# Kernel tuning notes

Hardware: AMD Instinct MI355X
Metric: run time of the kernel (lower is better)

## Reference

```python
import jax, jax.numpy as jnp
import numpy as np

D, T1, T2, T3 = 1024, 256, 128, 64
IV2, IV3, BUF = 16, 128, 32
B, T = 16, 1024

_PARAM_SHAPES = {
    "w_t1g": (D + T1, T1), "b_t1g": (T1,),
    "w_t1c": (D + T1, T1), "b_t1c": (T1,),
    "w_t1r": (T1, D), "b_t1r": (D,),
    "w_t2v": (D, T2), "b_t2v": (T2,),
    "w_t2b": (D, 1), "b_t2b": (1,),
    "w_t2r": (T2, D), "b_t2r": (D,),
    "w_t3o": (D, T3), "b_t3o": (T3,),
    "w_t3n": (D, T3), "b_t3n": (T3,),
    "w_t3r": (2 * T3, D), "b_t3r": (D,),
    "w_b32": (T3, T2), "b_b32": (T2,),
    "w_b21": (T2, T1), "b_b21": (T1,),
    "w_fuse": (3 * D, D), "b_fuse": (D,),
}

def setup_inputs() -> dict:
    key = jax.random.key(0)
    inp = {"x": jax.random.normal(jax.random.fold_in(key, 0), (B, T, D), jnp.float32)}
    for i, (name, shape) in enumerate(_PARAM_SHAPES.items()):
        inp[name] = 0.02 * jax.random.normal(jax.random.fold_in(key, i + 1), shape, jnp.float32)
    inp["ln_g"] = jnp.ones((D,), jnp.float32)
    inp["ln_b"] = jnp.zeros((D,), jnp.float32)
    return inp

def reference(x, w_t1g, b_t1g, w_t1c, b_t1c, w_t1r, b_t1r, w_t2v, b_t2v, w_t2b, b_t2b, w_t2r, b_t2r, w_t3o, b_t3o, w_t3n, b_t3n, w_t3r, b_t3r, w_b32, b_b32, w_b21, b_b21, w_fuse, b_fuse, ln_g, ln_b):
    Bsz, Tlen, _ = x.shape
    tier1 = jnp.zeros((Bsz, T1), x.dtype)
    tier2 = jnp.zeros((Bsz, T2), x.dtype)
    tier3 = jnp.zeros((Bsz, T3), x.dtype)
    var3 = jnp.ones((Bsz, T3), x.dtype)
    buf = jnp.zeros((Bsz, BUF, D), x.dtype)  # consolidation buffer

    def step(carry, inp_t):
        tier1, tier2, tier3, var3, buf = carry
        x_t, tc = inp_t  # tc = token_count (1-indexed)
        # cross-tier broadcasts
        bias21 = jnp.tanh(tier2 @ w_b21 + b_b21)
        bias32 = jnp.tanh(tier3 @ w_b32 + b_b32)
        # tier1: GRU-style gated update
        t1b = tier1 + bias21
        comb = jnp.concatenate([x_t, t1b], axis=-1)
        gate = jax.nn.sigmoid(comb @ w_t1g + b_t1g)
        cand = jnp.tanh(comb @ w_t1c + b_t1c)
        tier1 = gate * t1b + (1.0 - gate) * cand
        read1 = tier1 @ w_t1r + b_t1r
        # tier2: delta-rule overwrite every IV2 tokens (buffer mean BEFORE this token is written)
        do2 = (tc % IV2) == 0
        bm = buf.mean(axis=1)
        t2b = tier2 + bias32
        v = bm @ w_t2v + b_t2v
        beta = jax.nn.sigmoid(bm @ w_t2b + b_t2b)
        tier2 = jnp.where(do2, t2b + beta * (v - t2b), tier2)
        read2 = tier2 @ w_t2r + b_t2r
        # tier3: diagonal Kalman update every IV3 tokens, observation = tier2 readout
        do3 = (tc % IV3) == 0
        z = read2 @ w_t3o + b_t3o
        r = jax.nn.softplus(read2 @ w_t3n + b_t3n) + 0.01
        sp = 0.99 * var3 + 0.01
        K = sp / (sp + r + 1e-8)
        tier3 = jnp.where(do3, tier3 + K * (z - tier3), tier3)
        var3 = jnp.where(do3, (1.0 - K) * sp, var3)
        read3 = jnp.concatenate([tier3, var3], axis=-1) @ w_t3r + b_t3r
        fused = jnp.concatenate([read1, read2, read3], axis=-1) @ w_fuse + b_fuse
        # ring-buffer write (detached in torch -> stop_gradient)
        idx = (tc - 1) % BUF
        buf = jax.lax.dynamic_update_slice(buf, jax.lax.stop_gradient(x_t)[:, None, :], (0, idx, 0))
        return (tier1, tier2, tier3, var3, buf), fused

    tcs = jnp.arange(1, Tlen + 1, dtype=jnp.int32)
    _, ys = jax.lax.scan(step, (tier1, tier2, tier3, var3, buf), (jnp.swapaxes(x, 0, 1), tcs))
    out = jnp.swapaxes(ys, 0, 1)  # [B, T, D]
    mu = out.mean(-1, keepdims=True)
    xc = out - mu
    return xc * jax.lax.rsqrt(jnp.mean(xc * xc, -1, keepdims=True) + 1e-5) * ln_g + ln_b
```

## Files before the change

kernel.cpp:

```cpp
#include <hip/hip_runtime.h>

#define D_ 1024
#define T_ 1024
#define B_ 16

typedef short s16x8 __attribute__((ext_vector_type(8)));
typedef float f32x4 __attribute__((ext_vector_type(4)));

__device__ __forceinline__ unsigned short bf16_rne(float f){
  unsigned int u = __builtin_bit_cast(unsigned int, f);
  u += 0x7FFFu + ((u >> 16) & 1u);
  return (unsigned short)(u >> 16);
}
__device__ __forceinline__ float bf16_tof(unsigned short h){
  unsigned int u = ((unsigned int)h) << 16;
  return __builtin_bit_cast(float, u);
}
__device__ __forceinline__ float fsig(float x){ return 1.0f/(1.0f+__expf(-x)); }
__device__ __forceinline__ float ftanh(float x){ return 2.0f*fsig(2.0f*x)-1.0f; }

template <typename V>
__device__ __forceinline__ auto mfma_try(V a, V b, f32x4 c, int)
    -> decltype(__builtin_amdgcn_mfma_f32_16x16x32_bf16(a, b, c, 0, 0, 0)) {
  return __builtin_amdgcn_mfma_f32_16x16x32_bf16(a, b, c, 0, 0, 0);
}
template <typename V>
__device__ __forceinline__ f32x4 mfma_try(V a, V b, f32x4 c, long) {
  typedef __bf16 bf16x8 __attribute__((ext_vector_type(8)));
  return __builtin_amdgcn_mfma_f32_16x16x32_bf16(
      __builtin_bit_cast(bf16x8, a), __builtin_bit_cast(bf16x8, b), c, 0, 0, 0);
}
__device__ __forceinline__ f32x4 MFMA(s16x8 a, s16x8 b, f32x4 c){
  return mfma_try(a, b, c, 0);
}


__device__ __forceinline__ void dev_conv4(const float* __restrict__ s,
                                          unsigned short* __restrict__ d, int g){
  float4 v = *(const float4*)(s + (size_t)g*4);
  ushort4 o; o.x=bf16_rne(v.x); o.y=bf16_rne(v.y); o.z=bf16_rne(v.z); o.w=bf16_rne(v.w);
  *(ushort4*)(d + (size_t)g*4) = o;
}

__device__ __forceinline__ void dev_fragprep(const float* __restrict__ w, int rowOff,
                                             int KT, int Nsrc,
                                             unsigned short* __restrict__ dst, int slot){
  int lane = slot & 63; int tmp = slot >> 6; int kt = tmp % KT; int nt = tmp / KT;
  int kbase = kt*32 + (lane>>4)*8; int col = nt*16 + (lane&15);
  unsigned short* o = dst + (size_t)slot*8;
  #pragma unroll
  for (int j=0;j<8;j++) o[j] = bf16_rne(w[(size_t)(rowOff + kbase + j)*Nsrc + col]);
}

__device__ __forceinline__ void dev_bm(const float* __restrict__ x,
                                       unsigned short* __restrict__ bm, int blk, int tid){
  int e = blk >> 4; int b = blk & 15;
  int tc = 16*(e+1); int hi = tc-2; int lo = tc-33; if (lo < 0) lo = 0;
  const float* xb = x + (size_t)b*T_*D_;
  for (int d = tid; d < D_; d += 256){
    float s = 0.f;
    for (int ss = lo; ss <= hi; ++ss) s += xb[(size_t)ss*D_ + d];
    bm[((size_t)(e*16+b))*D_ + d] = bf16_rne(s * (1.0f/32.0f));
  }
}

__device__ __forceinline__ void dev_bconst(const float* __restrict__ wf, const float* __restrict__ bf,
                                           const float* __restrict__ b1, const float* __restrict__ b2,
                                           const float* __restrict__ b3, float* __restrict__ bc,
                                           int blk, int tid){
  __shared__ float part[4][64];
  int n = blk*64 + (tid&63);
  int sl = tid>>6;
  float s = 0.f;
  for (int k=sl*256; k<(sl+1)*256; ++k){
    s += b1[k]*wf[(size_t)k*1024+n] + b2[k]*wf[(size_t)(1024+k)*1024+n] + b3[k]*wf[(size_t)(2048+k)*1024+n];
  }
  part[sl][tid&63] = s; __syncthreads();
  if (sl==0) bc[n] = bf[n] + part[0][tid] + part[1][tid] + part[2][tid] + part[3][tid];
}

__device__ __forceinline__ void dev_b2(const float* __restrict__ b_t2r, const float* __restrict__ w3o,
                                       const float* __restrict__ b3o, const float* __restrict__ w3n,
                                       const float* __restrict__ b3n, float* __restrict__ b2o,
                                       float* __restrict__ b2n, int tid){
  __shared__ float part[2][128];
  int idx = tid & 127; int sl = tid >> 7;
  int mat = idx>>6, n = idx&63;
  const float* w = mat ? w3n : w3o;
  float s = 0.f;
  for (int k=sl*512; k<(sl+1)*512; ++k) s += b_t2r[k]*w[(size_t)k*64+n];
  part[sl][idx] = s; __syncthreads();
  if (sl==0){
    float r = part[0][idx] + part[1][idx] + (mat? b3n[n] : b3o[n]);
    if (mat) b2n[n] = r; else b2o[n] = r;
  }
}

__device__ __forceinline__ void dev_gemm(int M, int K,
    const unsigned short* __restrict__ A, int lda,
    const unsigned short* __restrict__ Bf,
    const float* __restrict__ bias, int act,
    float* __restrict__ C, int ldc, int cb, int rb, int tid){
  int KT = K >> 5;
  int w = tid >> 6, l = tid & 63;
  int rbase = rb*64 + w*16;
  int arow = rbase + (l & 15); if (arow >= M) arow = M-1;
  const unsigned short* Aptr = A + (size_t)arow*lda + ((l>>4)*8);
  const s16x8* B0 = (const s16x8*)Bf + ((size_t)(cb*4+0)*KT)*64 + l;
  const s16x8* B1 = (const s16x8*)Bf + ((size_t)(cb*4+1)*KT)*64 + l;
  const s16x8* B2 = (const s16x8*)Bf + ((size_t)(cb*4+2)*KT)*64 + l;
  const s16x8* B3 = (const s16x8*)Bf + ((size_t)(cb*4+3)*KT)*64 + l;
  f32x4 z = {0.f,0.f,0.f,0.f};
  f32x4 acc0=z, acc1=z, acc2=z, acc3=z;
  for (int kt=0; kt<KT; ++kt){
    s16x8 a = *(const s16x8*)(Aptr + (size_t)kt*32);
    acc0 = MFMA(a, B0[(size_t)kt*64], acc0);
    acc1 = MFMA(a, B1[(size_t)kt*64], acc1);
    acc2 = MFMA(a, B2[(size_t)kt*64], acc2);
    acc3 = MFMA(a, B3[(size_t)kt*64], acc3);
  }
  int r0 = (l>>4)*4;
  #pragma unroll
  for (int i=0;i<4;i++){
    f32x4 acc = i==0?acc0 : i==1?acc1 : i==2?acc2 : acc3;
    int col = (cb*4+i)*16 + (l&15);
    float bs = bias ? bias[col] : 0.0f;
    #pragma unroll
    for (int j=0;j<4;j++){
      int row = rbase + r0 + j;
      if (row < M){
        float vv = acc[j] + bs;
        if (act==1) vv = ftanh(vv);
        C[(size_t)row*ldc + col] = vv;
      }
    }
  }
}

__device__ void dev_traj(
    const float* __restrict__ v, const float* __restrict__ beta,
    const float* __restrict__ w_b32, const float* __restrict__ b_b32,
    const float* __restrict__ w2o, const float* __restrict__ b2o,
    const float* __restrict__ w2n, const float* __restrict__ b2n,
    unsigned short* __restrict__ t2traj, unsigned short* __restrict__ t3traj, int tid){
  __shared__ float t2[16*128];
  __shared__ float t3[16*64];
  __shared__ float var3[16*64];
  __shared__ float zb[16*64];
  __shared__ float rb[16*64];
  for (int i=tid;i<2048;i+=1024){ t2[i]=0.f; t2traj[i]=0; }
  for (int i=tid;i<1024;i+=1024){
    int b=i>>6, n=i&63;
    t3[i]=0.f; var3[i]=1.f;
    t3traj[(size_t)b*128 + n] = 0;
    t3traj[(size_t)b*128 + 64 + n] = bf16_rne(1.f);
  }
  __syncthreads();
  for (int k=1;k<=64;k++){
    for (int i=tid;i<2048;i+=1024){
      int b=i>>7, n=i&127;
      float s=b_b32[n];
      for (int j=0;j<64;j++) s += t3[b*64+j]*w_b32[j*128+n];
      float t2b = t2[i] + ftanh(s);
      float bt = beta[(k-1)*16+b];
      float nv = t2b + bt*(v[(size_t)((k-1)*16+b)*128+n] - t2b);
      t2[i]=nv;
      t2traj[((size_t)k*16+b)*128+n] = bf16_rne(nv);
    }
    if ((k&7)==0){
      __syncthreads();
      for (int i=tid;i<2048;i+=1024){
        int mat=i>>10, b=(i>>6)&15, n=i&63;
        const float* w = mat? w2n : w2o;
        float s = mat? b2n[n] : b2o[n];
        for (int j=0;j<128;j++) s += t2[b*128+j]*w[j*64+n];
        if (mat){ float r = (s>20.f)? s : log1pf(__expf(s)); rb[b*64+n]=r+0.01f; }
        else zb[b*64+n]=s;
      }
      __syncthreads();
      for (int i=tid;i<1024;i+=1024){
        int b=i>>6, n=i&63;
        float sp = 0.99f*var3[i]+0.01f;
        float Kk = sp/(sp+rb[i]+1e-8f);
        float t3n_ = t3[i] + Kk*(zb[i]-t3[i]);
        float v3n = (1.f-Kk)*sp;
        t3[i]=t3n_; var3[i]=v3n;
        int jj=k>>3;
        t3traj[((size_t)jj*16+b)*128+n]    = bf16_rne(t3n_);
        t3traj[((size_t)jj*16+b)*128+64+n] = bf16_rne(v3n);
      }
      __syncthreads();
    }
  }
}


__global__ __launch_bounds__(256) void k_f1(
    const float* __restrict__ x, unsigned short* __restrict__ xtb,
    const float* __restrict__ w_t1r, unsigned short* __restrict__ w_t1r_bf,
    const float* __restrict__ w_t2r, unsigned short* __restrict__ w_t2r_bf,
    const float* __restrict__ w_t3r, unsigned short* __restrict__ w_t3r_bf,
    const float* __restrict__ w_t1g, const float* __restrict__ w_t1c,
    unsigned short* __restrict__ wgc1f, unsigned short* __restrict__ wg2f,
    unsigned short* __restrict__ wc2f,
    const float* __restrict__ w_t2v, unsigned short* __restrict__ wtvf,
    const float* __restrict__ w_b21, unsigned short* __restrict__ wb21f,
    const float* __restrict__ w_fuse, unsigned short* __restrict__ wf1f,
    unsigned short* __restrict__ wf2f, unsigned short* __restrict__ wf3f,
    const float* __restrict__ w_t3o, unsigned short* __restrict__ w3of,
    const float* __restrict__ w_t3n, unsigned short* __restrict__ w3nf,
    unsigned short* __restrict__ bm,
    const float* __restrict__ b_fuse, const float* __restrict__ b_t1r,
    const float* __restrict__ b_t2r, const float* __restrict__ b_t3r,
    float* __restrict__ bconst,
    const float* __restrict__ b_t3o, const float* __restrict__ b_t3n,
    float* __restrict__ b2o, float* __restrict__ b2n,
    const float* __restrict__ b_t1g, const float* __restrict__ b_t1c,
    float* __restrict__ bgc){
  int blk = blockIdx.x, tid = threadIdx.x;
  if (blk < 1024){
    for (int i=0;i<16;i++){
      int r = blk*16 + i; int b = r & 15, t = r >> 4; int d = tid*4;
      float4 v = *(const float4*)(x + ((size_t)b*T_ + t)*D_ + d);
      ushort4 o; o.x=bf16_rne(v.x); o.y=bf16_rne(v.y); o.z=bf16_rne(v.z); o.w=bf16_rne(v.w);
      *(ushort4*)(xtb + (size_t)r*D_ + d) = o;
    }
  } else if (blk < 1280){ dev_conv4(w_t1r, w_t1r_bf, (blk-1024)*256 + tid); }
  else if (blk < 1408){ dev_conv4(w_t2r, w_t2r_bf, (blk-1280)*256 + tid); }
  else if (blk < 1536){ dev_conv4(w_t3r, w_t3r_bf, (blk-1408)*256 + tid); }
  else if (blk < 1664){ dev_fragprep(w_t1g, 0, 32, 256, wgc1f,          (blk-1536)*256 + tid); }
  else if (blk < 1792){ dev_fragprep(w_t1c, 0, 32, 256, wgc1f + 262144, (blk-1664)*256 + tid); }
  else if (blk < 1824){ dev_fragprep(w_t1g, 1024, 8, 256, wg2f, (blk-1792)*256 + tid); }
  else if (blk < 1856){ dev_fragprep(w_t1c, 1024, 8, 256, wc2f, (blk-1824)*256 + tid); }
  else if (blk < 1920){ dev_fragprep(w_t2v, 0, 32, 128, wtvf, (blk-1856)*256 + tid); }
  else if (blk < 1936){ dev_fragprep(w_b21, 0, 4, 256, wb21f, (blk-1920)*256 + tid); }
  else if (blk < 2448){ dev_fragprep(w_fuse, 0,    32, 1024, wf1f, (blk-1936)*256 + tid); }
  else if (blk < 2960){ dev_fragprep(w_fuse, 1024, 32, 1024, wf2f, (blk-2448)*256 + tid); }
  else if (blk < 3472){ dev_fragprep(w_fuse, 2048, 32, 1024, wf3f, (blk-2960)*256 + tid); }
  else if (blk < 3504){ dev_fragprep(w_t3o, 0, 32, 64, w3of, (blk-3472)*256 + tid); }
  else if (blk < 3536){ dev_fragprep(w_t3n, 0, 32, 64, w3nf, (blk-3504)*256 + tid); }
  else if (blk < 4560){ dev_bm(x, bm, blk-3536, tid); }
  else if (blk < 4576){ dev_bconst(w_fuse, b_fuse, b_t1r, b_t2r, b_t3r, bconst, blk-4560, tid); }
  else if (blk < 4577){ dev_b2(b_t2r, w_t3o, b_t3o, w_t3n, b_t3n, b2o, b2n, tid); }
  else { bgc[tid] = b_t1g[tid]; bgc[256+tid] = b_t1c[tid]; }
}

__global__ __launch_bounds__(256) void k_f2(
    const unsigned short* __restrict__ xtb, const unsigned short* __restrict__ wgc1f,
    const float* __restrict__ bgc, float* __restrict__ P,
    const unsigned short* __restrict__ bm, const unsigned short* __restrict__ wtvf,
    const float* __restrict__ b_t2v, float* __restrict__ v,
    const unsigned short* __restrict__ w_t1r_bf, const unsigned short* __restrict__ wf1f,
    float* __restrict__ wr1f,
    const unsigned short* __restrict__ w_t2r_bf, const unsigned short* __restrict__ wf2f,
    float* __restrict__ wr2f,
    const unsigned short* __restrict__ w_t3r_bf, const unsigned short* __restrict__ wf3f,
    float* __restrict__ wr3f,
    const unsigned short* __restrict__ w3of, float* __restrict__ w2o,
    const unsigned short* __restrict__ w3nf, float* __restrict__ w2n,
    const float* __restrict__ w_t2b, const float* __restrict__ b_t2b,
    float* __restrict__ beta){
  int blk = blockIdx.x, tid = threadIdx.x;
  if (blk < 2048){ int r = blk;        dev_gemm(16384, 1024, xtb, 1024, wgc1f, bgc, 0, P, 512, r&7, r>>3, tid); }
  else if (blk < 2080){ int r = blk-2048; dev_gemm(1024, 1024, bm, 1024, wtvf, b_t2v, 0, v, 128, r&1, r>>1, tid); }
  else if (blk < 2144){ int r = blk-2080; dev_gemm(256, 1024, w_t1r_bf, 1024, wf1f, nullptr, 0, wr1f, 1024, r&15, r>>4, tid); }
  else if (blk < 2176){ int r = blk-2144; dev_gemm(128, 1024, w_t2r_bf, 1024, wf2f, nullptr, 0, wr2f, 1024, r&15, r>>4, tid); }
  else if (blk < 2208){ int r = blk-2176; dev_gemm(128, 1024, w_t3r_bf, 1024, wf3f, nullptr, 0, wr3f, 1024, r&15, r>>4, tid); }
  else if (blk < 2210){ int r = blk-2208; dev_gemm(128, 1024, w_t2r_bf, 1024, w3of, nullptr, 0, w2o, 64, 0, r, tid); }
  else if (blk < 2212){ int r = blk-2210; dev_gemm(128, 1024, w_t2r_bf, 1024, w3nf, nullptr, 0, w2n, 64, 0, r, tid); }
  else {
    int rel = blk-2212;
    int r = rel*4 + (tid>>6), l = tid&63;
    float s = 0.f;
    for (int d=l; d<D_; d+=64) s += bf16_tof(bm[(size_t)r*D_+d]) * w_t2b[d];
    #pragma unroll
    for (int off=32; off; off>>=1) s += __shfl_down(s, off);
    if (l==0) beta[r] = fsig(s + b_t2b[0]);
  }
}

__global__ __launch_bounds__(1024) void k_f3(
    const float* __restrict__ wr1f, unsigned short* __restrict__ wr1ff,
    const float* __restrict__ wr2f, unsigned short* __restrict__ wr2ff,
    const float* __restrict__ wr3f, unsigned short* __restrict__ wr3ff,
    const float* __restrict__ v, const float* __restrict__ beta,
    const float* __restrict__ w_b32, const float* __restrict__ b_b32,
    const float* __restrict__ w2o, const float* __restrict__ b2o,
    const float* __restrict__ w2n, const float* __restrict__ b2n,
    unsigned short* __restrict__ t2traj, unsigned short* __restrict__ t3traj){
  int blk = blockIdx.x, tid = threadIdx.x;
  if (blk < 32){ dev_fragprep(wr1f, 0, 8, 1024, wr1ff, blk*1024 + tid); }
  else if (blk < 48){ dev_fragprep(wr2f, 0, 4, 1024, wr2ff, (blk-32)*1024 + tid); }
  else if (blk < 64){ dev_fragprep(wr3f, 0, 4, 1024, wr3ff, (blk-48)*1024 + tid); }
  else { dev_traj(v, beta, w_b32, b_b32, w2o, b2o, w2n, b2n, t2traj, t3traj, tid); }
}

__global__ __launch_bounds__(256) void k_f4(
    const unsigned short* __restrict__ t2traj, const unsigned short* __restrict__ wb21f,
    const float* __restrict__ b_b21, float* __restrict__ b21seg,
    const unsigned short* __restrict__ wr2ff, float* __restrict__ f2seg,
    const unsigned short* __restrict__ t3traj, const unsigned short* __restrict__ wr3ff,
    float* __restrict__ f3seg){
  int blk = blockIdx.x, tid = threadIdx.x;
  if (blk < 68){ int r = blk;      dev_gemm(1040, 128, t2traj, 128, wb21f, b_b21, 1, b21seg, 256, r&3, r>>2, tid); }
  else if (blk < 340){ int r = blk-68;  dev_gemm(1040, 128, t2traj, 128, wr2ff, nullptr, 0, f2seg, 1024, r&15, r>>4, tid); }
  else {               int r = blk-340; dev_gemm(144, 128, t3traj, 128, wr3ff, nullptr, 0, f3seg, 1024, r&15, r>>4, tid); }
}

__global__ __launch_bounds__(512) void k_recur(
    const float* __restrict__ P,
    const float* __restrict__ b21,
    const unsigned short* __restrict__ Wg2f, const unsigned short* __restrict__ Wc2f,
    unsigned short* __restrict__ traj){
  __shared__ unsigned short sbuf[2][256];
  int b = blockIdx.x;
  int tid = threadIdx.x, w = tid>>6, l = tid&63;
  int hi = l>>4, cl = l&15;
  const s16x8* Bg = (const s16x8*)Wg2f;
  const s16x8* Bc = (const s16x8*)Wc2f;
  s16x8 bg0[8], bg1[8], bc0[8], bc1[8];
  #pragma unroll
  for (int kt=0;kt<8;kt++){
    bg0[kt] = Bg[((size_t)(2*w)*8  +kt)*64 + l];
    bg1[kt] = Bg[((size_t)(2*w+1)*8+kt)*64 + l];
    bc0[kt] = Bc[((size_t)(2*w)*8  +kt)*64 + l];
    bc1[kt] = Bc[((size_t)(2*w+1)*8+kt)*64 + l];
  }
  bool owner = (hi < 2);
  int nt = 2*w + hi;
  int n  = nt*16 + cl;
  if (!owner) n = 2*w*16 + cl;
  float t1b = 0.f;
  float pgN=0.f, pcN=0.f, bbN=0.f;
  if (owner){
    bbN = b21[((size_t)b)*256 + n];
    t1b = bbN;
    pgN = P[((size_t)b)*512 + n];
    pcN = P[((size_t)b)*512 + 256 + n];
    sbuf[0][n] = bf16_rne(t1b);
  }
  asm volatile("s_waitcnt lgkmcnt(0)\ns_barrier" ::: "memory");
  for (int t=0;t<1024;t++){
    float pg = pgN, pc = pcN, bb = bbN;
    int tn = (t+1 < 1024) ? (t+1) : 1023;
    if (owner){
      pgN = P[((size_t)(tn*16+b))*512 + n];
      pcN = P[((size_t)(tn*16+b))*512 + 256 + n];
      bbN = b21[(((size_t)((t+2)>>4))*16 + b)*256 + n];
    }
    const unsigned short* sb = sbuf[t&1];
    f32x4 z = {0.f,0.f,0.f,0.f};
    f32x4 ag0=z, ag1=z, ac0=z, ac1=z;
    #pragma unroll
    for (int kt=0;kt<8;kt++){
      s16x8 a = *(const s16x8*)(sb + kt*32 + hi*8);
      ag0 = MFMA(a, bg0[kt], ag0);
      ag1 = MFMA(a, bg1[kt], ag1);
      ac0 = MFMA(a, bc0[kt], ac0);
      ac1 = MFMA(a, bc1[kt], ac1);
    }
    if (owner){
      float gacc = (hi==0)? ag0[0] : ag1[0];
      float cacc = (hi==0)? ac0[0] : ac1[0];
      float g = fsig(gacc + pg);
      float c = ftanh(cacc + pc);
      float t1n = g*t1b + (1.f-g)*c;
      traj[((size_t)(t*16+b))*256 + n] = bf16_rne(t1n);
      t1b = t1n + bb;
      sbuf[(t+1)&1][n] = bf16_rne(t1b);
    }
    asm volatile("s_waitcnt lgkmcnt(0)\ns_barrier" ::: "memory");
  }
}

__global__ __launch_bounds__(1024) void k_final(
    const unsigned short* __restrict__ traj, const unsigned short* __restrict__ Bf,
    const float* __restrict__ bconst, const float* __restrict__ f2seg, const float* __restrict__ f3seg,
    const float* __restrict__ ln_g, const float* __restrict__ ln_b, float* __restrict__ out){
  __shared__ float buf[16*1024];
  __shared__ float mu[16];
  __shared__ float rs[16];
  int t = blockIdx.x, tid = threadIdx.x, w = tid>>6, l = tid&63;
  const unsigned short* Ab = traj + ((size_t)t*16 + (l&15))*256 + (l>>4)*8;
  const s16x8* Bp = (const s16x8*)Bf;
  f32x4 z = {0.f,0.f,0.f,0.f};
  f32x4 ac[4]; ac[0]=z; ac[1]=z; ac[2]=z; ac[3]=z;
  #pragma unroll
  for (int kt=0;kt<8;kt++){
    s16x8 a = *(const s16x8*)(Ab + kt*32);
    #pragma unroll
    for (int i=0;i<4;i++){
      int nt = w*4+i;
      ac[i] = MFMA(a, Bp[((size_t)nt*8+kt)*64+l], ac[i]);
    }
  }
  int tc = t+1, s2 = tc>>4, s3 = tc>>7;
  int r0 = (l>>4)*4, cl = l&15;
  #pragma unroll
  for (int i=0;i<4;i++){
    int col = (w*4+i)*16+cl;
    #pragma unroll
    for (int j=0;j<4;j++){
      int b = r0+j;
      buf[b*1024+col] = ac[i][j] + bconst[col]
        + f2seg[((size_t)s2*16+b)*1024+col] + f3seg[((size_t)s3*16+b)*1024+col];
    }
  }
  __syncthreads();
  {
    float s=0.f, q=0.f;
    #pragma unroll
    for (int i=0;i<16;i++){ float xv = buf[w*1024 + l + 64*i]; s+=xv; q+=xv*xv; }
    #pragma unroll
    for (int off=32;off;off>>=1){ s += __shfl_down(s,off); q += __shfl_down(q,off); }
    if (l==0){ float m = s*(1.f/1024.f); float var = q*(1.f/1024.f) - m*m; mu[w]=m; rs[w]=rsqrtf(var+1e-5f); }
  }
  __syncthreads();
  {
    int b = tid>>6, d0 = tid&63;
    float m = mu[b], r = rs[b];
    size_t ob = ((size_t)b*1024 + t)*1024;
    #pragma unroll
    for (int i=0;i<16;i++){
      int d = d0 + 64*i;
      out[ob + d] = (buf[b*1024+d]-m)*r*ln_g[d] + ln_b[d];
    }
  }
}

extern "C" void kernel_launch(void* const* d_in, const int* in_sizes, int n_in,
                              void* d_out, int out_size, void* d_ws, size_t ws_size,
                              hipStream_t stream){
  const float* x     = (const float*)d_in[0];
  const float* w_t1g = (const float*)d_in[1];
  const float* b_t1g = (const float*)d_in[2];
  const float* w_t1c = (const float*)d_in[3];
  const float* b_t1c = (const float*)d_in[4];
  const float* w_t1r = (const float*)d_in[5];
  const float* b_t1r = (const float*)d_in[6];
  const float* w_t2v = (const float*)d_in[7];
  const float* b_t2v = (const float*)d_in[8];
  const float* w_t2b = (const float*)d_in[9];
  const float* b_t2b = (const float*)d_in[10];
  const float* w_t2r = (const float*)d_in[11];
  const float* b_t2r = (const float*)d_in[12];
  const float* w_t3o = (const float*)d_in[13];
  const float* b_t3o = (const float*)d_in[14];
  const float* w_t3n = (const float*)d_in[15];
  const float* b_t3n = (const float*)d_in[16];
  const float* w_t3r = (const float*)d_in[17];
  const float* b_t3r = (const float*)d_in[18];
  const float* w_b32 = (const float*)d_in[19];
  const float* b_b32 = (const float*)d_in[20];
  const float* w_b21 = (const float*)d_in[21];
  const float* b_b21 = (const float*)d_in[22];
  const float* w_fuse= (const float*)d_in[23];
  const float* b_fuse= (const float*)d_in[24];
  const float* ln_g  = (const float*)d_in[25];
  const float* ln_b  = (const float*)d_in[26];
  float* out = (float*)d_out;
  (void)in_sizes; (void)n_in; (void)out_size; (void)ws_size;

  char* base = (char*)d_ws;
  size_t off = 0;
  auto alloc = [&](size_t bytes) -> void* {
    void* p = base + off;
    off += (bytes + 255) & ~(size_t)255;
    return p;
  };
  unsigned short* xtb   = (unsigned short*)alloc((size_t)B_*T_*D_*2);
  float* P              = (float*)alloc((size_t)B_*T_*512*4);
  unsigned short* traj1 = (unsigned short*)alloc((size_t)B_*T_*256*2);
  unsigned short* bm    = (unsigned short*)alloc((size_t)1024*1024*2);
  float* v      = (float*)alloc((size_t)1024*128*4);
  float* beta   = (float*)alloc(1024*4);
  float* wr1f   = (float*)alloc((size_t)256*1024*4);
  float* wr2f   = (float*)alloc((size_t)128*1024*4);
  float* wr3f   = (float*)alloc((size_t)128*1024*4);
  float* w2o    = (float*)alloc(128*64*4);
  float* w2n    = (float*)alloc(128*64*4);
  float* b2o    = (float*)alloc(64*4);
  float* b2n    = (float*)alloc(64*4);
  float* bconst = (float*)alloc(1024*4);
  float* bgc    = (float*)alloc(512*4);
  unsigned short* t2traj = (unsigned short*)alloc((size_t)1040*128*2);
  unsigned short* t3traj = (unsigned short*)alloc((size_t)144*128*2);
  float* b21seg = (float*)alloc((size_t)1040*256*4);
  float* f2seg  = (float*)alloc((size_t)1040*1024*4);
  float* f3seg  = (float*)alloc((size_t)144*1024*4);
  unsigned short* w_t1r_bf = (unsigned short*)alloc((size_t)256*1024*2);
  unsigned short* w_t2r_bf = (unsigned short*)alloc((size_t)128*1024*2);
  unsigned short* w_t3r_bf = (unsigned short*)alloc((size_t)128*1024*2);
  unsigned short* wgc1f = (unsigned short*)alloc((size_t)1024*512*2);
  unsigned short* wg2f  = (unsigned short*)alloc((size_t)256*256*2);
  unsigned short* wc2f  = (unsigned short*)alloc((size_t)256*256*2);
  unsigned short* wtvf  = (unsigned short*)alloc((size_t)1024*128*2);
  unsigned short* wb21f = (unsigned short*)alloc((size_t)128*256*2);
  unsigned short* wf1f  = (unsigned short*)alloc((size_t)1024*1024*2);
  unsigned short* wf2f  = (unsigned short*)alloc((size_t)1024*1024*2);
  unsigned short* wf3f  = (unsigned short*)alloc((size_t)1024*1024*2);
  unsigned short* w3of  = (unsigned short*)alloc((size_t)1024*64*2);
  unsigned short* w3nf  = (unsigned short*)alloc((size_t)1024*64*2);
  unsigned short* wr1ff = (unsigned short*)alloc((size_t)256*1024*2);
  unsigned short* wr2ff = (unsigned short*)alloc((size_t)128*1024*2);
  unsigned short* wr3ff = (unsigned short*)alloc((size_t)128*1024*2);

  k_f1<<<dim3(4578), dim3(256), 0, stream>>>(
      x, xtb, w_t1r, w_t1r_bf, w_t2r, w_t2r_bf, w_t3r, w_t3r_bf,
      w_t1g, w_t1c, wgc1f, wg2f, wc2f, w_t2v, wtvf, w_b21, wb21f,
      w_fuse, wf1f, wf2f, wf3f, w_t3o, w3of, w_t3n, w3nf, bm,
      b_fuse, b_t1r, b_t2r, b_t3r, bconst, b_t3o, b_t3n, b2o, b2n,
      b_t1g, b_t1c, bgc);
  k_f2<<<dim3(2468), dim3(256), 0, stream>>>(
      xtb, wgc1f, bgc, P, bm, wtvf, b_t2v, v,
      w_t1r_bf, wf1f, wr1f, w_t2r_bf, wf2f, wr2f, w_t3r_bf, wf3f, wr3f,
      w3of, w2o, w3nf, w2n, w_t2b, b_t2b, beta);
  k_f3<<<dim3(65), dim3(1024), 0, stream>>>(
      wr1f, wr1ff, wr2f, wr2ff, wr3f, wr3ff,
      v, beta, w_b32, b_b32, w2o, b2o, w2n, b2n, t2traj, t3traj);
  k_f4<<<dim3(388), dim3(256), 0, stream>>>(
      t2traj, wb21f, b_b21, b21seg, wr2ff, f2seg, t3traj, wr3ff, f3seg);
  k_recur<<<dim3(16), dim3(512), 0, stream>>>(P, b21seg, wg2f, wc2f, traj1);
  k_final<<<dim3(1024), dim3(1024), 0, stream>>>(traj1, wr1ff, bconst, f2seg, f3seg, ln_g, ln_b, out);
}
```

Baseline: 1.311 ms.

## Overlap tier2/3 readout GEMMs with tier1 recurrence, widen recurrence blocks

The f2seg/f3seg readout GEMMs move out of k_f4 into extra blocks of k_recur, so they run alongside the 16 serial recurrence blocks instead of ahead of them. The recurrence now uses 1024 threads, with each wave owning one 16-column tile of the gate and candidate weights, which halves the MFMA chain per wave per step. The tier2/3 trajectory loop hoists the bias32 tanh matvec out of the inner step, since tier3 only changes every 8 steps. The risk is that the co-scheduled GEMM blocks compete with the latency-bound recurrence for the same compute units, and that 1024-thread barriers cost more per step.

```diff
diff --git a/kernel.cpp b/kernel.cpp
--- a/kernel.cpp
+++ b/kernel.cpp
@@ -100,10 +100,10 @@
     const unsigned short* __restrict__ A, int lda,
     const unsigned short* __restrict__ Bf,
     const float* __restrict__ bias, int act,
-    float* __restrict__ C, int ldc, int cb, int rb, int tid){
+    float* __restrict__ C, int ldc, int cb, int rb, int tid, int rows){
   int KT = K >> 5;
   int w = tid >> 6, l = tid & 63;
-  int rbase = rb*64 + w*16;
+  int rbase = rb*rows + w*16;
   int arow = rbase + (l & 15); if (arow >= M) arow = M-1;
   const unsigned short* Aptr = A + (size_t)arow*lda + ((l>>4)*8);
   const s16x8* B0 = (const s16x8*)Bf + ((size_t)(cb*4+0)*KT)*64 + l;
@@ -148,6 +148,7 @@
   __shared__ float var3[16*64];
   __shared__ float zb[16*64];
   __shared__ float rb[16*64];
+  __shared__ float b32[16*128];
   for (int i=tid;i<2048;i+=1024){ t2[i]=0.f; t2traj[i]=0; }
   for (int i=tid;i<1024;i+=1024){
     int b=i>>6, n=i&63;
@@ -156,41 +157,46 @@
     t3traj[(size_t)b*128 + 64 + n] = bf16_rne(1.f);
   }
   __syncthreads();
-  for (int k=1;k<=64;k++){
+  for (int g=0; g<8; ++g){
     for (int i=tid;i<2048;i+=1024){
       int b=i>>7, n=i&127;
       float s=b_b32[n];
       for (int j=0;j<64;j++) s += t3[b*64+j]*w_b32[j*128+n];
-      float t2b = t2[i] + ftanh(s);
-      float bt = beta[(k-1)*16+b];
-      float nv = t2b + bt*(v[(size_t)((k-1)*16+b)*128+n] - t2b);
-      t2[i]=nv;
-      t2traj[((size_t)k*16+b)*128+n] = bf16_rne(nv);
-    }
-    if ((k&7)==0){
-      __syncthreads();
+      b32[i] = ftanh(s);
+    }
+    __syncthreads();
+    for (int kk=0; kk<8; ++kk){
+      int k = g*8 + kk + 1;
       for (int i=tid;i<2048;i+=1024){
-        int mat=i>>10, b=(i>>6)&15, n=i&63;
-        const float* w = mat? w2n : w2o;
-        float s = mat? b2n[n] : b2o[n];
-        for (int j=0;j<128;j++) s += t2[b*128+j]*w[j*64+n];
-        if (mat){ float r = (s>20.f)? s : log1pf(__expf(s)); rb[b*64+n]=r+0.01f; }
-        else zb[b*64+n]=s;
+        int b=i>>7, n=i&127;
+        float t2b = t2[i] + b32[i];
+        float bt = beta[(k-1)*16+b];
+        float nv = t2b + bt*(v[(size_t)((k-1)*16+b)*128+n] - t2b);
+        t2[i]=nv;
+        t2traj[((size_t)k*16+b)*128+n] = bf16_rne(nv);
       }
-      __syncthreads();
-      for (int i=tid;i<1024;i+=1024){
-        int b=i>>6, n=i&63;
-        float sp = 0.99f*var3[i]+0.01f;
-        float Kk = sp/(sp+rb[i]+1e-8f);
-        float t3n_ = t3[i] + Kk*(zb[i]-t3[i]);
-        float v3n = (1.f-Kk)*sp;
-        t3[i]=t3n_; var3[i]=v3n;
-        int jj=k>>3;
-        t3traj[((size_t)jj*16+b)*128+n]    = bf16_rne(t3n_);
-        t3traj[((size_t)jj*16+b)*128+64+n] = bf16_rne(v3n);
-      }
-      __syncthreads();
-    }
+    }
+    __syncthreads();
+    for (int i=tid;i<2048;i+=1024){
+      int mat=i>>10, b=(i>>6)&15, n=i&63;
+      const float* w = mat? w2n : w2o;
+      float s = mat? b2n[n] : b2o[n];
+      for (int j=0;j<128;j++) s += t2[b*128+j]*w[j*64+n];
+      if (mat){ float r = (s>20.f)? s : log1pf(__expf(s)); rb[b*64+n]=r+0.01f; }
+      else zb[b*64+n]=s;
+    }
+    __syncthreads();
+    for (int i=tid;i<1024;i+=1024){
+      int b=i>>6, n=i&63;
+      float sp = 0.99f*var3[i]+0.01f;
+      float Kk = sp/(sp+rb[i]+1e-8f);
+      float t3n_ = t3[i] + Kk*(zb[i]-t3[i]);
+      float v3n = (1.f-Kk)*sp;
+      t3[i]=t3n_; var3[i]=v3n;
+      t3traj[((size_t)(g+1)*16+b)*128+n]    = bf16_rne(t3n_);
+      t3traj[((size_t)(g+1)*16+b)*128+64+n] = bf16_rne(v3n);
+    }
+    __syncthreads();
   }
 }
 
@@ -261,13 +267,13 @@
     const float* __restrict__ w_t2b, const float* __restrict__ b_t2b,
     float* __restrict__ beta){
   int blk = blockIdx.x, tid = threadIdx.x;
-  if (blk < 2048){ int r = blk;        dev_gemm(16384, 1024, xtb, 1024, wgc1f, bgc, 0, P, 512, r&7, r>>3, tid); }
-  else if (blk < 2080){ int r = blk-2048; dev_gemm(1024, 1024, bm, 1024, wtvf, b_t2v, 0, v, 128, r&1, r>>1, tid); }
-  else if (blk < 2144){ int r = blk-2080; dev_gemm(256, 1024, w_t1r_bf, 1024, wf1f, nullptr, 0, wr1f, 1024, r&15, r>>4, tid); }
-  else if (blk < 2176){ int r = blk-2144; dev_gemm(128, 1024, w_t2r_bf, 1024, wf2f, nullptr, 0, wr2f, 1024, r&15, r>>4, tid); }
-  else if (blk < 2208){ int r = blk-2176; dev_gemm(128, 1024, w_t3r_bf, 1024, wf3f, nullptr, 0, wr3f, 1024, r&15, r>>4, tid); }
-  else if (blk < 2210){ int r = blk-2208; dev_gemm(128, 1024, w_t2r_bf, 1024, w3of, nullptr, 0, w2o, 64, 0, r, tid); }
-  else if (blk < 2212){ int r = blk-2210; dev_gemm(128, 1024, w_t2r_bf, 1024, w3nf, nullptr, 0, w2n, 64, 0, r, tid); }
+  if (blk < 2048){ int r = blk;        dev_gemm(16384, 1024, xtb, 1024, wgc1f, bgc, 0, P, 512, r&7, r>>3, tid, 64); }
+  else if (blk < 2080){ int r = blk-2048; dev_gemm(1024, 1024, bm, 1024, wtvf, b_t2v, 0, v, 128, r&1, r>>1, tid, 64); }
+  else if (blk < 2144){ int r = blk-2080; dev_gemm(256, 1024, w_t1r_bf, 1024, wf1f, nullptr, 0, wr1f, 1024, r&15, r>>4, tid, 64); }
+  else if (blk < 2176){ int r = blk-2144; dev_gemm(128, 1024, w_t2r_bf, 1024, wf2f, nullptr, 0, wr2f, 1024, r&15, r>>4, tid, 64); }
+  else if (blk < 2208){ int r = blk-2176; dev_gemm(128, 1024, w_t3r_bf, 1024, wf3f, nullptr, 0, wr3f, 1024, r&15, r>>4, tid, 64); }
+  else if (blk < 2210){ int r = blk-2208; dev_gemm(128, 1024, w_t2r_bf, 1024, w3of, nullptr, 0, w2o, 64, 0, r, tid, 64); }
+  else if (blk < 2212){ int r = blk-2210; dev_gemm(128, 1024, w_t2r_bf, 1024, w3nf, nullptr, 0, w2n, 64, 0, r, tid, 64); }
   else {
     int rel = blk-2212;
     int r = rel*4 + (tid>>6), l = tid&63;
@@ -297,39 +303,41 @@
 
 __global__ __launch_bounds__(256) void k_f4(
     const unsigned short* __restrict__ t2traj, const unsigned short* __restrict__ wb21f,
-    const float* __restrict__ b_b21, float* __restrict__ b21seg,
-    const unsigned short* __restrict__ wr2ff, float* __restrict__ f2seg,
-    const unsigned short* __restrict__ t3traj, const unsigned short* __restrict__ wr3ff,
-    float* __restrict__ f3seg){
+    const float* __restrict__ b_b21, float* __restrict__ b21seg){
   int blk = blockIdx.x, tid = threadIdx.x;
-  if (blk < 68){ int r = blk;      dev_gemm(1040, 128, t2traj, 128, wb21f, b_b21, 1, b21seg, 256, r&3, r>>2, tid); }
-  else if (blk < 340){ int r = blk-68;  dev_gemm(1040, 128, t2traj, 128, wr2ff, nullptr, 0, f2seg, 1024, r&15, r>>4, tid); }
-  else {               int r = blk-340; dev_gemm(144, 128, t3traj, 128, wr3ff, nullptr, 0, f3seg, 1024, r&15, r>>4, tid); }
-}
-
-__global__ __launch_bounds__(512) void k_recur(
+  dev_gemm(1040, 128, t2traj, 128, wb21f, b_b21, 1, b21seg, 256, blk&3, blk>>2, tid, 64);
+}
+
+__global__ __launch_bounds__(1024, 1) void k_recur(
     const float* __restrict__ P,
     const float* __restrict__ b21,
     const unsigned short* __restrict__ Wg2f, const unsigned short* __restrict__ Wc2f,
-    unsigned short* __restrict__ traj){
+    unsigned short* __restrict__ traj,
+    const unsigned short* __restrict__ t2traj, const unsigned short* __restrict__ wr2ff,
+    float* __restrict__ f2seg,
+    const unsigned short* __restrict__ t3traj, const unsigned short* __restrict__ wr3ff,
+    float* __restrict__ f3seg){
   __shared__ unsigned short sbuf[2][256];
-  int b = blockIdx.x;
-  int tid = threadIdx.x, w = tid>>6, l = tid&63;
+  int blk = blockIdx.x, tid = threadIdx.x;
+  if (blk >= 16){
+    int rel = blk - 16;
+    if (rel < 80) dev_gemm(1040, 128, t2traj, 128, wr2ff, nullptr, 0, f2seg, 1024, rel&15, rel>>4, tid, 256);
+    else          dev_gemm(144,  128, t3traj, 128, wr3ff, nullptr, 0, f3seg, 1024, rel-80, 0,     tid, 256);
+    return;
+  }
+  int b = blk;
+  int w = tid>>6, l = tid&63;
   int hi = l>>4, cl = l&15;
   const s16x8* Bg = (const s16x8*)Wg2f;
   const s16x8* Bc = (const s16x8*)Wc2f;
-  s16x8 bg0[8], bg1[8], bc0[8], bc1[8];
+  s16x8 bg[8], bc[8];
   #pragma unroll
   for (int kt=0;kt<8;kt++){
-    bg0[kt] = Bg[((size_t)(2*w)*8  +kt)*64 + l];
-    bg1[kt] = Bg[((size_t)(2*w+1)*8+kt)*64 + l];
-    bc0[kt] = Bc[((size_t)(2*w)*8  +kt)*64 + l];
-    bc1[kt] = Bc[((size_t)(2*w+1)*8+kt)*64 + l];
-  }
-  bool owner = (hi < 2);
-  int nt = 2*w + hi;
-  int n  = nt*16 + cl;
-  if (!owner) n = 2*w*16 + cl;
+    bg[kt] = Bg[((size_t)(w*8+kt))*64 + l];
+    bc[kt] = Bc[((size_t)(w*8+kt))*64 + l];
+  }
+  bool owner = (hi == 0);
+  int n = w*16 + cl;
   float t1b = 0.f;
   float pgN=0.f, pcN=0.f, bbN=0.f;
   if (owner){
@@ -350,20 +358,16 @@
     }
     const unsigned short* sb = sbuf[t&1];
     f32x4 z = {0.f,0.f,0.f,0.f};
-    f32x4 ag0=z, ag1=z, ac0=z, ac1=z;
+    f32x4 ag=z, ac=z;
     #pragma unroll
     for (int kt=0;kt<8;kt++){
       s16x8 a = *(const s16x8*)(sb + kt*32 + hi*8);
-      ag0 = MFMA(a, bg0[kt], ag0);
-      ag1 = MFMA(a, bg1[kt], ag1);
-      ac0 = MFMA(a, bc0[kt], ac0);
-      ac1 = MFMA(a, bc1[kt], ac1);
+      ag = MFMA(a, bg[kt], ag);
+      ac = MFMA(a, bc[kt], ac);
     }
     if (owner){
-      float gacc = (hi==0)? ag0[0] : ag1[0];
-      float cacc = (hi==0)? ac0[0] : ac1[0];
-      float g = fsig(gacc + pg);
-      float c = ftanh(cacc + pc);
+      float g = fsig(ag[0] + pg);
+      float c = ftanh(ac[0] + pc);
       float t1n = g*t1b + (1.f-g)*c;
       traj[((size_t)(t*16+b))*256 + n] = bf16_rne(t1n);
       t1b = t1n + bb;
@@ -518,8 +522,9 @@
   k_f3<<<dim3(65), dim3(1024), 0, stream>>>(
       wr1f, wr1ff, wr2f, wr2ff, wr3f, wr3ff,
       v, beta, w_b32, b_b32, w2o, b2o, w2n, b2n, t2traj, t3traj);
-  k_f4<<<dim3(388), dim3(256), 0, stream>>>(
-      t2traj, wb21f, b_b21, b21seg, wr2ff, f2seg, t3traj, wr3ff, f3seg);
-  k_recur<<<dim3(16), dim3(512), 0, stream>>>(P, b21seg, wg2f, wc2f, traj1);
+  k_f4<<<dim3(68), dim3(256), 0, stream>>>(t2traj, wb21f, b_b21, b21seg);
+  k_recur<<<dim3(112), dim3(1024), 0, stream>>>(
+      P, b21seg, wg2f, wc2f, traj1,
+      t2traj, wr2ff, f2seg, t3traj, wr3ff, f3seg);
   k_final<<<dim3(1024), dim3(1024), 0, stream>>>(traj1, wr1ff, bconst, f2seg, f3seg, ln_g, ln_b, out);
 }
```

Measured after the change: 1.137 ms. 13.3% less time.
